# Kernel optimization log

Measured on AMD Instinct MI355X. Metric: run time of the kernel, lower is better.

The kernel has to match this reference:

```python
import jax, jax.numpy as jnp
import numpy as np

B, S, D, H = 2, 2048, 1024, 16
DH = D // H  # depth per head = 64


def setup_inputs() -> dict:
    key = jax.random.key(0)
    ks = jax.random.split(key, 5)
    sc = 0.02
    return {
        "x": jax.random.normal(ks[0], (B, S, D), dtype=jnp.float32),
        "Wq": jax.random.normal(ks[1], (D, D), dtype=jnp.float32) * sc,
        "bq": jnp.zeros((D,), dtype=jnp.float32),
        "Wk": jax.random.normal(ks[2], (D, D), dtype=jnp.float32) * sc,
        "bk": jnp.zeros((D,), dtype=jnp.float32),
        "Wv": jax.random.normal(ks[3], (D, D), dtype=jnp.float32) * sc,
        "bv": jnp.zeros((D,), dtype=jnp.float32),
        "Wo": jax.random.normal(ks[4], (D, D), dtype=jnp.float32) * sc,
        "bo": jnp.zeros((D,), dtype=jnp.float32),
    }


def _split_heads(t):
    # [B,S,D] -> [B,H,S,DH]
    return t.reshape(B, S, H, DH).transpose(0, 2, 1, 3)


def reference(x, Wq, bq, Wk, bk, Wv, bv, Wo, bo):
    q = _split_heads(x @ Wq + bq)
    k = _split_heads(x @ Wk + bk)
    v = _split_heads(x @ Wv + bv)
    scale = 1.0 / jnp.sqrt(jnp.float32(DH))
    logits = jnp.einsum("bhqd,bhkd->bhqk", q, k) * scale  # [B,H,S,S]
    attn = jax.nn.softmax(logits, axis=-1)
    ctx = jnp.einsum("bhqk,bhkd->bhqd", attn, v)
    ctx = ctx.transpose(0, 2, 1, 3).reshape(B, S, D)
    # dropout is identity at inference
    return ctx @ Wo + bo
```

## Files before the change

kernel.cpp:

```cpp
#include <hip/hip_runtime.h>
#include <hip/hip_bf16.h>

#define S_LEN   2048
#define D_MODEL 1024
#define NHEAD   16
#define DHEAD   64
#define M_ROWS  4096
#define BHEADS  32

typedef __attribute__((ext_vector_type(8)))  short short8;
typedef __attribute__((ext_vector_type(4)))  float f32x4;
typedef __attribute__((ext_vector_type(16))) float f32x16;
typedef __attribute__((ext_vector_type(4)))  unsigned short us4;

extern "C" __device__ float __ocml_native_exp2_f32(float);

__device__ __forceinline__ unsigned short f2b(float f) {
    unsigned int u = __builtin_bit_cast(unsigned int, f);
    return (unsigned short)((u + 0x7FFFu + ((u >> 16) & 1u)) >> 16);
}

__device__ __forceinline__ unsigned int pk2b(float lo, float hi) {
    unsigned int u0 = __builtin_bit_cast(unsigned int, lo) + 0x8000u;
    unsigned int u1 = __builtin_bit_cast(unsigned int, hi) + 0x8000u;
    return __builtin_amdgcn_perm(u1, u0, 0x07060302u);
}

#define GLOAD16(gp, lp) __builtin_amdgcn_global_load_lds(                     \
        (const __attribute__((address_space(1))) void*)(gp),                  \
        (__attribute__((address_space(3))) void*)(lp), 16, 0, 0)

#define STAGE_OFS(lane) ((((lane) & 3) ^ (((lane) >> 3) & 3)) * 8)

__global__ __launch_bounds__(256) void convert_x(
    const float* __restrict__ x, unsigned short* __restrict__ xb)
{
    const int i = (blockIdx.x * 256 + threadIdx.x) * 4;
    const float4 v = *(const float4*)&x[i];
    us4 o;
    o.x = f2b(v.x); o.y = f2b(v.y); o.z = f2b(v.z); o.w = f2b(v.w);
    *(us4*)&xb[i] = o;
}

__global__ __launch_bounds__(256) void transpose_w(
    const float* __restrict__ Wq, const float* __restrict__ Wk,
    const float* __restrict__ Wv, const float* __restrict__ Wo,
    unsigned short* __restrict__ Wqt, unsigned short* __restrict__ Wkt,
    unsigned short* __restrict__ Wvt, unsigned short* __restrict__ Wot)
{
    __shared__ float tile[32][33];
    const int z = blockIdx.z;
    const float* W = z == 0 ? Wq : (z == 1 ? Wk : (z == 2 ? Wv : Wo));
    unsigned short* Wt = z == 0 ? Wqt : (z == 1 ? Wkt : (z == 2 ? Wvt : Wot));
    const int tx = threadIdx.x, ty = threadIdx.y;
    const int n0 = blockIdx.x * 32, k0 = blockIdx.y * 32;
    #pragma unroll
    for (int i = 0; i < 4; ++i)
        tile[ty + i * 8][tx] = W[(size_t)(k0 + ty + i * 8) * D_MODEL + n0 + tx];
    __syncthreads();
    #pragma unroll
    for (int i = 0; i < 4; ++i)
        Wt[(size_t)(n0 + ty + i * 8) * D_MODEL + k0 + tx] = f2b(tile[tx][ty + i * 8]);
}

__global__ __launch_bounds__(256) void gemm_qkv(
    const unsigned short* __restrict__ xb,
    const unsigned short* __restrict__ Wqt, const unsigned short* __restrict__ Wkt,
    const unsigned short* __restrict__ Wvt,
    const float* __restrict__ bq, const float* __restrict__ bk,
    const float* __restrict__ bv,
    unsigned short* __restrict__ Qb, unsigned short* __restrict__ Kb,
    unsigned short* __restrict__ Vt)
{
    __shared__ unsigned short As[128][32];
    __shared__ unsigned short Bs[128][32];

    const int z = blockIdx.z;
    const unsigned short* Wt = z == 0 ? Wqt : (z == 1 ? Wkt : Wvt);
    const float* bias = z == 0 ? bq : (z == 1 ? bk : bv);

    const int t = threadIdx.x, lane = t & 63, w = t >> 6;
    const int wm = w >> 1, wn = w & 1;
    const int bm = blockIdx.y * 128, bn = blockIdx.x * 128;
    const int lr = lane >> 2, lc = STAGE_OFS(lane);
    const int lm = lane & 15, quad = lane >> 4;
    const int qo = (quad ^ ((lm >> 1) & 3)) * 8;

    f32x4 acc[4][4] = {};

    for (int kt = 0; kt < D_MODEL; kt += 32) {
        __syncthreads();
        #pragma unroll
        for (int i = 0; i < 2; ++i) {
            const int c = 2 * w + i;
            GLOAD16(xb + (size_t)(bm + c * 16 + lr) * D_MODEL + kt + lc, &As[c * 16][0]);
            GLOAD16(Wt + (size_t)(bn + c * 16 + lr) * D_MODEL + kt + lc, &Bs[c * 16][0]);
        }
        __syncthreads();

        short8 af[4], bfr[4];
        #pragma unroll
        for (int mi = 0; mi < 4; ++mi)
            af[mi] = *(const short8*)&As[wm * 64 + mi * 16 + lm][qo];
        #pragma unroll
        for (int ni = 0; ni < 4; ++ni)
            bfr[ni] = *(const short8*)&Bs[wn * 64 + ni * 16 + lm][qo];
        #pragma unroll
        for (int mi = 0; mi < 4; ++mi)
            #pragma unroll
            for (int ni = 0; ni < 4; ++ni)
                acc[mi][ni] = __builtin_amdgcn_mfma_f32_16x16x32_bf16(
                    af[mi], bfr[ni], acc[mi][ni], 0, 0, 0);
    }

    float bb[4];
    #pragma unroll
    for (int ni = 0; ni < 4; ++ni)
        bb[ni] = bias[bn + wn * 64 + ni * 16 + lm];
    const float scale = (z == 0) ? 0.18033688011112042f : 1.0f;

    if (z < 2) {
        unsigned short* Out = (z == 0) ? Qb : Kb;
        #pragma unroll
        for (int mi = 0; mi < 4; ++mi)
            #pragma unroll
            for (int r = 0; r < 4; ++r) {
                const int row = bm + wm * 64 + mi * 16 + quad * 4 + r;
                const int b = row >> 11, s = row & 2047;
                #pragma unroll
                for (int ni = 0; ni < 4; ++ni) {
                    const int col = bn + wn * 64 + ni * 16 + lm;
                    const int h = col >> 6, d = col & 63;
                    Out[(((size_t)(b * NHEAD + h)) * S_LEN + s) * DHEAD + d] =
                        f2b((acc[mi][ni][r] + bb[ni]) * scale);
                }
            }
    } else {
        #pragma unroll
        for (int mi = 0; mi < 4; ++mi) {
            const int row0 = bm + wm * 64 + mi * 16 + quad * 4;
            const int b = row0 >> 11, s0 = row0 & 2047;
            #pragma unroll
            for (int ni = 0; ni < 4; ++ni) {
                const int col = bn + wn * 64 + ni * 16 + lm;
                const int h = col >> 6, d = col & 63;
                us4 pk;
                pk.x = f2b(acc[mi][ni][0] + bb[ni]);
                pk.y = f2b(acc[mi][ni][1] + bb[ni]);
                pk.z = f2b(acc[mi][ni][2] + bb[ni]);
                pk.w = f2b(acc[mi][ni][3] + bb[ni]);
                *(us4*)&Vt[(((size_t)(b * NHEAD + h)) * DHEAD + d) * S_LEN + s0] = pk;
            }
        }
    }
}

__global__ __launch_bounds__(256) void gemm_out(
    const unsigned short* __restrict__ Ab, const unsigned short* __restrict__ Wot,
    const float* __restrict__ bo, float* __restrict__ out)
{
    __shared__ unsigned short As[64][32];
    __shared__ unsigned short Bs[128][32];

    const int t = threadIdx.x, lane = t & 63, w = t >> 6;
    const int wm = w & 1, wn = w >> 1;
    const int bm = blockIdx.y * 64, bn = blockIdx.x * 128;
    const int lr = lane >> 2, lc = STAGE_OFS(lane);
    const int lm = lane & 15, quad = lane >> 4;
    const int qo = (quad ^ ((lm >> 1) & 3)) * 8;

    f32x4 acc[2][4] = {};

    for (int kt = 0; kt < D_MODEL; kt += 32) {
        __syncthreads();
        GLOAD16(Ab + (size_t)(bm + w * 16 + lr) * D_MODEL + kt + lc, &As[w * 16][0]);
        #pragma unroll
        for (int i = 0; i < 2; ++i)
            GLOAD16(Wot + (size_t)(bn + w * 32 + i * 16 + lr) * D_MODEL + kt + lc,
                    &Bs[w * 32 + i * 16][0]);
        __syncthreads();

        short8 af[2], bfr[4];
        #pragma unroll
        for (int mi = 0; mi < 2; ++mi)
            af[mi] = *(const short8*)&As[wm * 32 + mi * 16 + lm][qo];
        #pragma unroll
        for (int ni = 0; ni < 4; ++ni)
            bfr[ni] = *(const short8*)&Bs[wn * 64 + ni * 16 + lm][qo];
        #pragma unroll
        for (int mi = 0; mi < 2; ++mi)
            #pragma unroll
            for (int ni = 0; ni < 4; ++ni)
                acc[mi][ni] = __builtin_amdgcn_mfma_f32_16x16x32_bf16(
                    af[mi], bfr[ni], acc[mi][ni], 0, 0, 0);
    }

    float bb[4];
    #pragma unroll
    for (int ni = 0; ni < 4; ++ni)
        bb[ni] = bo[bn + wn * 64 + ni * 16 + lm];

    #pragma unroll
    for (int mi = 0; mi < 2; ++mi)
        #pragma unroll
        for (int r = 0; r < 4; ++r) {
            const int row = bm + wm * 32 + mi * 16 + quad * 4 + r;
            #pragma unroll
            for (int ni = 0; ni < 4; ++ni) {
                const int col = bn + wn * 64 + ni * 16 + lm;
                out[(size_t)row * D_MODEL + col] = acc[mi][ni][r] + bb[ni];
            }
        }
}

__global__ __launch_bounds__(256) void attn_mfma(
    const unsigned short* __restrict__ Q, const unsigned short* __restrict__ K,
    const unsigned short* __restrict__ V, unsigned short* __restrict__ Cx)
{
    __shared__ unsigned short Qs[2][128][32];
    __shared__ unsigned short Ks[2][64][32];
    __shared__ unsigned short Vs[2][64][32];
    __shared__ unsigned int   Ps[4][32][36];

    const int t = threadIdx.x, lane = t & 63, w = t >> 6;
    const int q5 = lane & 31, hi = lane >> 5;
    const int lr = lane >> 2, lcs = STAGE_OFS(lane);
    const int q0 = blockIdx.x * 128, bh = blockIdx.y;
    const int sw = (q5 >> 1) & 3;
    int sbo[4];
    #pragma unroll
    for (int sb = 0; sb < 4; ++sb) sbo[sb] = (sb ^ sw) * 8;

    const unsigned short* Qh = Q + (size_t)bh * (S_LEN * DHEAD);
    const unsigned short* Kh = K + (size_t)bh * (S_LEN * DHEAD);
    const unsigned short* Vh = V + (size_t)bh * (DHEAD * S_LEN);

    #pragma unroll
    for (int i = 0; i < 2; ++i)
        #pragma unroll
        for (int c = 0; c < 2; ++c)
            GLOAD16(Qh + (size_t)(q0 + w * 32 + c * 16 + lr) * DHEAD + i * 32 + lcs,
                    &Qs[i][w * 32 + c * 16][0]);
    __syncthreads();

    short8 qf[4];
    #pragma unroll
    for (int c = 0; c < 4; ++c)
        qf[c] = *(const short8*)&Qs[c >> 1][w * 32 + q5][sbo[(c & 1) * 2 + hi]];

    f32x16 acc[2] = {};
    float2 l2a = {0.f, 0.f}, l2b = {0.f, 0.f};

    for (int kt = 0; kt < S_LEN; kt += 64) {
        __syncthreads();
        #pragma unroll
        for (int i = 0; i < 2; ++i) {
            GLOAD16(Kh + (size_t)(kt + w * 16 + lr) * DHEAD + i * 32 + lcs,
                    &Ks[i][w * 16][0]);
            GLOAD16(Vh + (size_t)(w * 16 + lr) * S_LEN + kt + i * 32 + lcs,
                    &Vs[i][w * 16][0]);
        }
        __syncthreads();

        f32x16 sf[2] = {};
        #pragma unroll
        for (int c = 0; c < 4; ++c) {
            #pragma unroll
            for (int mt = 0; mt < 2; ++mt) {
                const short8 kf =
                    *(const short8*)&Ks[c >> 1][mt * 32 + q5][sbo[(c & 1) * 2 + hi]];
                sf[mt] = __builtin_amdgcn_mfma_f32_32x32x16_bf16(kf, qf[c], sf[mt], 0, 0, 0);
            }
        }

        #pragma unroll
        for (int mt = 0; mt < 2; ++mt)
            #pragma unroll
            for (int g = 0; g < 4; ++g) {
                const float p0 = __ocml_native_exp2_f32(sf[mt][g * 4 + 0]);
                const float p1 = __ocml_native_exp2_f32(sf[mt][g * 4 + 1]);
                const float p2 = __ocml_native_exp2_f32(sf[mt][g * 4 + 2]);
                const float p3 = __ocml_native_exp2_f32(sf[mt][g * 4 + 3]);
                l2a.x += p0; l2a.y += p1;
                l2b.x += p2; l2b.y += p3;
                uint2 pk;
                pk.x = pk2b(p0, p1);
                pk.y = pk2b(p2, p3);
                *(uint2*)&Ps[w][q5][mt * 16 + g * 4 + hi * 2] = pk;
            }

        #pragma unroll
        for (int c = 0; c < 4; ++c) {
            const short8 pf = *(const short8*)&Ps[w][q5][c * 8 + hi * 4];
            #pragma unroll
            for (int nt = 0; nt < 2; ++nt) {
                const short8 vf =
                    *(const short8*)&Vs[c >> 1][nt * 32 + q5][sbo[(c & 1) * 2 + hi]];
                acc[nt] = __builtin_amdgcn_mfma_f32_32x32x16_bf16(pf, vf, acc[nt], 0, 0, 0);
            }
        }
    }

    float l_acc = (l2a.x + l2a.y) + (l2b.x + l2b.y);
    l_acc += __shfl_xor(l_acc, 32);
    const float inv = 1.f / l_acc;
    const int b = bh >> 4, h = bh & 15;
    #pragma unroll
    for (int reg = 0; reg < 16; ++reg) {
        const int row = (reg & 3) + 8 * (reg >> 2) + 4 * hi;
        const float invr = __shfl(inv, row);
        const int s = q0 + w * 32 + row;
        const size_t base = ((size_t)(b * S_LEN + s)) * D_MODEL + h * DHEAD;
        Cx[base + q5]      = f2b(acc[0][reg] * invr);
        Cx[base + 32 + q5] = f2b(acc[1][reg] * invr);
    }
}

extern "C" void kernel_launch(void* const* d_in, const int* in_sizes, int n_in,
                              void* d_out, int out_size, void* d_ws, size_t ws_size,
                              hipStream_t stream)
{
    const float* x  = (const float*)d_in[0];
    const float* Wq = (const float*)d_in[1];
    const float* bq = (const float*)d_in[2];
    const float* Wk = (const float*)d_in[3];
    const float* bk = (const float*)d_in[4];
    const float* Wv = (const float*)d_in[5];
    const float* bv = (const float*)d_in[6];
    const float* Wo = (const float*)d_in[7];
    const float* bo = (const float*)d_in[8];
    float* out = (float*)d_out;

    unsigned short* xb  = (unsigned short*)d_ws;
    unsigned short* Wqt = xb  + (size_t)M_ROWS * D_MODEL;
    unsigned short* Wkt = Wqt + (size_t)D_MODEL * D_MODEL;
    unsigned short* Wvt = Wkt + (size_t)D_MODEL * D_MODEL;
    unsigned short* Wot = Wvt + (size_t)D_MODEL * D_MODEL;
    unsigned short* Qb  = Wot + (size_t)D_MODEL * D_MODEL;
    unsigned short* Kb  = Qb  + (size_t)M_ROWS * D_MODEL;
    unsigned short* Vt  = Kb  + (size_t)M_ROWS * D_MODEL;
    unsigned short* Cxb = Vt  + (size_t)M_ROWS * D_MODEL;

    convert_x<<<dim3(M_ROWS * D_MODEL / 1024), dim3(256), 0, stream>>>(x, xb);
    transpose_w<<<dim3(32, 32, 4), dim3(32, 8), 0, stream>>>(
        Wq, Wk, Wv, Wo, Wqt, Wkt, Wvt, Wot);

    gemm_qkv<<<dim3(D_MODEL / 128, M_ROWS / 128, 3), dim3(256), 0, stream>>>(
        xb, Wqt, Wkt, Wvt, bq, bk, bv, Qb, Kb, Vt);

    attn_mfma<<<dim3(S_LEN / 128, BHEADS), dim3(256), 0, stream>>>(Qb, Kb, Vt, Cxb);

    gemm_out<<<dim3(D_MODEL / 128, M_ROWS / 64), dim3(256), 0, stream>>>(
        Cxb, Wot, bo, out);
}
```

Measured before the change: 210.1 us.

## Merge prep kernels and pass attention probabilities via lane shuffles instead of LDS

Folds the x-to-bf16 conversion into the weight transpose kernel as an extra grid slice, saving one kernel launch. In attention, the softmax probabilities are packed into registers and exchanged across half-waves with shuffles to form the PV MFMA operand. This removes the per-warp LDS buffer and its store/load round trip. Also adds a min-blocks-per-CU hint of 4 to the attention kernel, which could force register spilling.

```diff
diff --git a/kernel.cpp b/kernel.cpp
--- a/kernel.cpp
+++ b/kernel.cpp
@@ -32,27 +32,31 @@
 
 #define STAGE_OFS(lane) ((((lane) & 3) ^ (((lane) >> 3) & 3)) * 8)
 
-__global__ __launch_bounds__(256) void convert_x(
-    const float* __restrict__ x, unsigned short* __restrict__ xb)
-{
-    const int i = (blockIdx.x * 256 + threadIdx.x) * 4;
-    const float4 v = *(const float4*)&x[i];
-    us4 o;
-    o.x = f2b(v.x); o.y = f2b(v.y); o.z = f2b(v.z); o.w = f2b(v.w);
-    *(us4*)&xb[i] = o;
-}
-
-__global__ __launch_bounds__(256) void transpose_w(
+__global__ __launch_bounds__(256) void prep(
+    const float* __restrict__ x, unsigned short* __restrict__ xb,
     const float* __restrict__ Wq, const float* __restrict__ Wk,
     const float* __restrict__ Wv, const float* __restrict__ Wo,
     unsigned short* __restrict__ Wqt, unsigned short* __restrict__ Wkt,
     unsigned short* __restrict__ Wvt, unsigned short* __restrict__ Wot)
 {
+    const int z = blockIdx.z;
+    const int tx = threadIdx.x, ty = threadIdx.y;
+    if (z == 4) {
+        const int blk = blockIdx.y * 32 + blockIdx.x;
+        const int base = (blk * 256 + ty * 32 + tx) * 4;
+        #pragma unroll
+        for (int r = 0; r < 4; ++r) {
+            const int i = base + r * (M_ROWS * D_MODEL / 4);
+            const float4 v = *(const float4*)&x[i];
+            us4 o;
+            o.x = f2b(v.x); o.y = f2b(v.y); o.z = f2b(v.z); o.w = f2b(v.w);
+            *(us4*)&xb[i] = o;
+        }
+        return;
+    }
     __shared__ float tile[32][33];
-    const int z = blockIdx.z;
     const float* W = z == 0 ? Wq : (z == 1 ? Wk : (z == 2 ? Wv : Wo));
     unsigned short* Wt = z == 0 ? Wqt : (z == 1 ? Wkt : (z == 2 ? Wvt : Wot));
-    const int tx = threadIdx.x, ty = threadIdx.y;
     const int n0 = blockIdx.x * 32, k0 = blockIdx.y * 32;
     #pragma unroll
     for (int i = 0; i < 4; ++i)
@@ -213,14 +217,13 @@
         }
 }
 
-__global__ __launch_bounds__(256) void attn_mfma(
+__global__ __launch_bounds__(256, 4) void attn_mfma(
     const unsigned short* __restrict__ Q, const unsigned short* __restrict__ K,
     const unsigned short* __restrict__ V, unsigned short* __restrict__ Cx)
 {
     __shared__ unsigned short Qs[2][128][32];
     __shared__ unsigned short Ks[2][64][32];
     __shared__ unsigned short Vs[2][64][32];
-    __shared__ unsigned int   Ps[4][32][36];
 
     const int t = threadIdx.x, lane = t & 63, w = t >> 6;
     const int q5 = lane & 31, hi = lane >> 5;
@@ -274,29 +277,35 @@
         }
 
         #pragma unroll
-        for (int mt = 0; mt < 2; ++mt)
-            #pragma unroll
-            for (int g = 0; g < 4; ++g) {
-                const float p0 = __ocml_native_exp2_f32(sf[mt][g * 4 + 0]);
-                const float p1 = __ocml_native_exp2_f32(sf[mt][g * 4 + 1]);
-                const float p2 = __ocml_native_exp2_f32(sf[mt][g * 4 + 2]);
-                const float p3 = __ocml_native_exp2_f32(sf[mt][g * 4 + 3]);
+        for (int mt = 0; mt < 2; ++mt) {
+            unsigned int D[4][2];
+            #pragma unroll
+            for (int b = 0; b < 4; ++b) {
+                const float p0 = __ocml_native_exp2_f32(sf[mt][b * 4 + 0]);
+                const float p1 = __ocml_native_exp2_f32(sf[mt][b * 4 + 1]);
+                const float p2 = __ocml_native_exp2_f32(sf[mt][b * 4 + 2]);
+                const float p3 = __ocml_native_exp2_f32(sf[mt][b * 4 + 3]);
                 l2a.x += p0; l2a.y += p1;
                 l2b.x += p2; l2b.y += p3;
-                uint2 pk;
-                pk.x = pk2b(p0, p1);
-                pk.y = pk2b(p2, p3);
-                *(uint2*)&Ps[w][q5][mt * 16 + g * 4 + hi * 2] = pk;
-            }
-
-        #pragma unroll
-        for (int c = 0; c < 4; ++c) {
-            const short8 pf = *(const short8*)&Ps[w][q5][c * 8 + hi * 4];
-            #pragma unroll
-            for (int nt = 0; nt < 2; ++nt) {
-                const short8 vf =
-                    *(const short8*)&Vs[c >> 1][nt * 32 + q5][sbo[(c & 1) * 2 + hi]];
-                acc[nt] = __builtin_amdgcn_mfma_f32_32x32x16_bf16(pf, vf, acc[nt], 0, 0, 0);
+                D[b][0] = pk2b(p0, p1);
+                D[b][1] = pk2b(p2, p3);
+            }
+            #pragma unroll
+            for (int h01 = 0; h01 < 2; ++h01) {
+                const unsigned int sx0 = __shfl_xor(D[2 * h01 + (hi ^ 1)][0], 32);
+                const unsigned int sx1 = __shfl_xor(D[2 * h01 + (hi ^ 1)][1], 32);
+                uint4 fr;
+                fr.x = hi ? sx0 : D[2 * h01][0];
+                fr.y = hi ? sx1 : D[2 * h01][1];
+                fr.z = hi ? D[2 * h01 + 1][0] : sx0;
+                fr.w = hi ? D[2 * h01 + 1][1] : sx1;
+                const short8 pf = __builtin_bit_cast(short8, fr);
+                #pragma unroll
+                for (int nt = 0; nt < 2; ++nt) {
+                    const short8 vf =
+                        *(const short8*)&Vs[mt][nt * 32 + q5][sbo[h01 * 2 + hi]];
+                    acc[nt] = __builtin_amdgcn_mfma_f32_32x32x16_bf16(pf, vf, acc[nt], 0, 0, 0);
+                }
             }
         }
     }
@@ -341,9 +350,8 @@
     unsigned short* Vt  = Kb  + (size_t)M_ROWS * D_MODEL;
     unsigned short* Cxb = Vt  + (size_t)M_ROWS * D_MODEL;
 
-    convert_x<<<dim3(M_ROWS * D_MODEL / 1024), dim3(256), 0, stream>>>(x, xb);
-    transpose_w<<<dim3(32, 32, 4), dim3(32, 8), 0, stream>>>(
-        Wq, Wk, Wv, Wo, Wqt, Wkt, Wvt, Wot);
+    prep<<<dim3(32, 32, 5), dim3(32, 8), 0, stream>>>(
+        x, xb, Wq, Wk, Wv, Wo, Wqt, Wkt, Wvt, Wot);
 
     gemm_qkv<<<dim3(D_MODEL / 128, M_ROWS / 128, 3), dim3(256), 0, stream>>>(
         xb, Wqt, Wkt, Wvt, bq, bk, bv, Qb, Kb, Vt);
```

Result: slower. 218.1 us (+3.8%).

## Double-buffer LDS tiles in GEMMs and attention, merge prep kernels

Applied to the files above, without the earlier changes.

The two GEMM kernels and the attention kernel now double-buffer their shared-memory tiles. The next K-slice is issued with global_load_lds before the MFMAs on the current buffer run, and each iteration ends with one barrier instead of two. The x conversion and weight transposes are merged into one prep launch, using a fifth grid slice for x, to save one kernel launch. This doubles LDS use per block, which may cut occupancy. Correctness relies on the single end-of-iteration barrier also covering completion of the async LDS loads.

```diff
diff --git a/kernel.cpp b/kernel.cpp
--- a/kernel.cpp
+++ b/kernel.cpp
@@ -32,27 +32,31 @@
 
 #define STAGE_OFS(lane) ((((lane) & 3) ^ (((lane) >> 3) & 3)) * 8)
 
-__global__ __launch_bounds__(256) void convert_x(
-    const float* __restrict__ x, unsigned short* __restrict__ xb)
-{
-    const int i = (blockIdx.x * 256 + threadIdx.x) * 4;
-    const float4 v = *(const float4*)&x[i];
-    us4 o;
-    o.x = f2b(v.x); o.y = f2b(v.y); o.z = f2b(v.z); o.w = f2b(v.w);
-    *(us4*)&xb[i] = o;
-}
-
-__global__ __launch_bounds__(256) void transpose_w(
+__global__ __launch_bounds__(256) void prep(
+    const float* __restrict__ x, unsigned short* __restrict__ xb,
     const float* __restrict__ Wq, const float* __restrict__ Wk,
     const float* __restrict__ Wv, const float* __restrict__ Wo,
     unsigned short* __restrict__ Wqt, unsigned short* __restrict__ Wkt,
     unsigned short* __restrict__ Wvt, unsigned short* __restrict__ Wot)
 {
+    const int z = blockIdx.z;
+    const int tx = threadIdx.x, ty = threadIdx.y;
+    if (z == 4) {
+        const int blk = blockIdx.y * 32 + blockIdx.x;
+        const int base = (blk * 256 + ty * 32 + tx) * 4;
+        #pragma unroll
+        for (int r = 0; r < 4; ++r) {
+            const int i = base + r * (M_ROWS * D_MODEL / 4);
+            const float4 v = *(const float4*)&x[i];
+            us4 o;
+            o.x = f2b(v.x); o.y = f2b(v.y); o.z = f2b(v.z); o.w = f2b(v.w);
+            *(us4*)&xb[i] = o;
+        }
+        return;
+    }
     __shared__ float tile[32][33];
-    const int z = blockIdx.z;
     const float* W = z == 0 ? Wq : (z == 1 ? Wk : (z == 2 ? Wv : Wo));
     unsigned short* Wt = z == 0 ? Wqt : (z == 1 ? Wkt : (z == 2 ? Wvt : Wot));
-    const int tx = threadIdx.x, ty = threadIdx.y;
     const int n0 = blockIdx.x * 32, k0 = blockIdx.y * 32;
     #pragma unroll
     for (int i = 0; i < 4; ++i)
@@ -72,8 +76,8 @@
     unsigned short* __restrict__ Qb, unsigned short* __restrict__ Kb,
     unsigned short* __restrict__ Vt)
 {
-    __shared__ unsigned short As[128][32];
-    __shared__ unsigned short Bs[128][32];
+    __shared__ unsigned short As[2][128][32];
+    __shared__ unsigned short Bs[2][128][32];
 
     const int z = blockIdx.z;
     const unsigned short* Wt = z == 0 ? Wqt : (z == 1 ? Wkt : Wvt);
@@ -88,29 +92,43 @@
 
     f32x4 acc[4][4] = {};
 
-    for (int kt = 0; kt < D_MODEL; kt += 32) {
-        __syncthreads();
-        #pragma unroll
-        for (int i = 0; i < 2; ++i) {
-            const int c = 2 * w + i;
-            GLOAD16(xb + (size_t)(bm + c * 16 + lr) * D_MODEL + kt + lc, &As[c * 16][0]);
-            GLOAD16(Wt + (size_t)(bn + c * 16 + lr) * D_MODEL + kt + lc, &Bs[c * 16][0]);
-        }
-        __syncthreads();
+    #pragma unroll
+    for (int i = 0; i < 2; ++i) {
+        const int c = 2 * w + i;
+        GLOAD16(xb + (size_t)(bm + c * 16 + lr) * D_MODEL + lc, &As[0][c * 16][0]);
+        GLOAD16(Wt + (size_t)(bn + c * 16 + lr) * D_MODEL + lc, &Bs[0][c * 16][0]);
+    }
+    __syncthreads();
+
+    for (int it = 0; it < 32; ++it) {
+        const int cur = it & 1;
+        if (it + 1 < 32) {
+            const int kt = (it + 1) * 32;
+            #pragma unroll
+            for (int i = 0; i < 2; ++i) {
+                const int c = 2 * w + i;
+                GLOAD16(xb + (size_t)(bm + c * 16 + lr) * D_MODEL + kt + lc,
+                        &As[cur ^ 1][c * 16][0]);
+                GLOAD16(Wt + (size_t)(bn + c * 16 + lr) * D_MODEL + kt + lc,
+                        &Bs[cur ^ 1][c * 16][0]);
+            }
+        }
 
         short8 af[4], bfr[4];
         #pragma unroll
         for (int mi = 0; mi < 4; ++mi)
-            af[mi] = *(const short8*)&As[wm * 64 + mi * 16 + lm][qo];
+            af[mi] = *(const short8*)&As[cur][wm * 64 + mi * 16 + lm][qo];
         #pragma unroll
         for (int ni = 0; ni < 4; ++ni)
-            bfr[ni] = *(const short8*)&Bs[wn * 64 + ni * 16 + lm][qo];
+            bfr[ni] = *(const short8*)&Bs[cur][wn * 64 + ni * 16 + lm][qo];
         #pragma unroll
         for (int mi = 0; mi < 4; ++mi)
             #pragma unroll
             for (int ni = 0; ni < 4; ++ni)
                 acc[mi][ni] = __builtin_amdgcn_mfma_f32_16x16x32_bf16(
                     af[mi], bfr[ni], acc[mi][ni], 0, 0, 0);
+
+        __syncthreads();
     }
 
     float bb[4];
@@ -159,8 +177,8 @@
     const unsigned short* __restrict__ Ab, const unsigned short* __restrict__ Wot,
     const float* __restrict__ bo, float* __restrict__ out)
 {
-    __shared__ unsigned short As[64][32];
-    __shared__ unsigned short Bs[128][32];
+    __shared__ unsigned short As[2][64][32];
+    __shared__ unsigned short Bs[2][128][32];
 
     const int t = threadIdx.x, lane = t & 63, w = t >> 6;
     const int wm = w & 1, wn = w >> 1;
@@ -171,28 +189,40 @@
 
     f32x4 acc[2][4] = {};
 
-    for (int kt = 0; kt < D_MODEL; kt += 32) {
-        __syncthreads();
-        GLOAD16(Ab + (size_t)(bm + w * 16 + lr) * D_MODEL + kt + lc, &As[w * 16][0]);
-        #pragma unroll
-        for (int i = 0; i < 2; ++i)
-            GLOAD16(Wot + (size_t)(bn + w * 32 + i * 16 + lr) * D_MODEL + kt + lc,
-                    &Bs[w * 32 + i * 16][0]);
-        __syncthreads();
+    GLOAD16(Ab + (size_t)(bm + w * 16 + lr) * D_MODEL + lc, &As[0][w * 16][0]);
+    #pragma unroll
+    for (int i = 0; i < 2; ++i)
+        GLOAD16(Wot + (size_t)(bn + w * 32 + i * 16 + lr) * D_MODEL + lc,
+                &Bs[0][w * 32 + i * 16][0]);
+    __syncthreads();
+
+    for (int it = 0; it < 32; ++it) {
+        const int cur = it & 1;
+        if (it + 1 < 32) {
+            const int kt = (it + 1) * 32;
+            GLOAD16(Ab + (size_t)(bm + w * 16 + lr) * D_MODEL + kt + lc,
+                    &As[cur ^ 1][w * 16][0]);
+            #pragma unroll
+            for (int i = 0; i < 2; ++i)
+                GLOAD16(Wot + (size_t)(bn + w * 32 + i * 16 + lr) * D_MODEL + kt + lc,
+                        &Bs[cur ^ 1][w * 32 + i * 16][0]);
+        }
 
         short8 af[2], bfr[4];
         #pragma unroll
         for (int mi = 0; mi < 2; ++mi)
-            af[mi] = *(const short8*)&As[wm * 32 + mi * 16 + lm][qo];
+            af[mi] = *(const short8*)&As[cur][wm * 32 + mi * 16 + lm][qo];
         #pragma unroll
         for (int ni = 0; ni < 4; ++ni)
-            bfr[ni] = *(const short8*)&Bs[wn * 64 + ni * 16 + lm][qo];
+            bfr[ni] = *(const short8*)&Bs[cur][wn * 64 + ni * 16 + lm][qo];
         #pragma unroll
         for (int mi = 0; mi < 2; ++mi)
             #pragma unroll
             for (int ni = 0; ni < 4; ++ni)
                 acc[mi][ni] = __builtin_amdgcn_mfma_f32_16x16x32_bf16(
                     af[mi], bfr[ni], acc[mi][ni], 0, 0, 0);
+
+        __syncthreads();
     }
 
     float bb[4];
@@ -218,8 +248,8 @@
     const unsigned short* __restrict__ V, unsigned short* __restrict__ Cx)
 {
     __shared__ unsigned short Qs[2][128][32];
-    __shared__ unsigned short Ks[2][64][32];
-    __shared__ unsigned short Vs[2][64][32];
+    __shared__ unsigned short Ks[2][2][64][32];
+    __shared__ unsigned short Vs[2][2][64][32];
     __shared__ unsigned int   Ps[4][32][36];
 
     const int t = threadIdx.x, lane = t & 63, w = t >> 6;
@@ -241,6 +271,11 @@
         for (int c = 0; c < 2; ++c)
             GLOAD16(Qh + (size_t)(q0 + w * 32 + c * 16 + lr) * DHEAD + i * 32 + lcs,
                     &Qs[i][w * 32 + c * 16][0]);
+    #pragma unroll
+    for (int i = 0; i < 2; ++i) {
+        GLOAD16(Kh + (size_t)(w * 16 + lr) * DHEAD + i * 32 + lcs, &Ks[0][i][w * 16][0]);
+        GLOAD16(Vh + (size_t)(w * 16 + lr) * S_LEN + i * 32 + lcs, &Vs[0][i][w * 16][0]);
+    }
     __syncthreads();
 
     short8 qf[4];
@@ -251,16 +286,18 @@
     f32x16 acc[2] = {};
     float2 l2a = {0.f, 0.f}, l2b = {0.f, 0.f};
 
-    for (int kt = 0; kt < S_LEN; kt += 64) {
-        __syncthreads();
-        #pragma unroll
-        for (int i = 0; i < 2; ++i) {
-            GLOAD16(Kh + (size_t)(kt + w * 16 + lr) * DHEAD + i * 32 + lcs,
-                    &Ks[i][w * 16][0]);
-            GLOAD16(Vh + (size_t)(w * 16 + lr) * S_LEN + kt + i * 32 + lcs,
-                    &Vs[i][w * 16][0]);
-        }
-        __syncthreads();
+    for (int it = 0; it < 32; ++it) {
+        const int cur = it & 1;
+        if (it + 1 < 32) {
+            const int kt = (it + 1) * 64;
+            #pragma unroll
+            for (int i = 0; i < 2; ++i) {
+                GLOAD16(Kh + (size_t)(kt + w * 16 + lr) * DHEAD + i * 32 + lcs,
+                        &Ks[cur ^ 1][i][w * 16][0]);
+                GLOAD16(Vh + (size_t)(w * 16 + lr) * S_LEN + kt + i * 32 + lcs,
+                        &Vs[cur ^ 1][i][w * 16][0]);
+            }
+        }
 
         f32x16 sf[2] = {};
         #pragma unroll
@@ -268,7 +305,7 @@
             #pragma unroll
             for (int mt = 0; mt < 2; ++mt) {
                 const short8 kf =
-                    *(const short8*)&Ks[c >> 1][mt * 32 + q5][sbo[(c & 1) * 2 + hi]];
+                    *(const short8*)&Ks[cur][c >> 1][mt * 32 + q5][sbo[(c & 1) * 2 + hi]];
                 sf[mt] = __builtin_amdgcn_mfma_f32_32x32x16_bf16(kf, qf[c], sf[mt], 0, 0, 0);
             }
         }
@@ -295,10 +332,12 @@
             #pragma unroll
             for (int nt = 0; nt < 2; ++nt) {
                 const short8 vf =
-                    *(const short8*)&Vs[c >> 1][nt * 32 + q5][sbo[(c & 1) * 2 + hi]];
+                    *(const short8*)&Vs[cur][c >> 1][nt * 32 + q5][sbo[(c & 1) * 2 + hi]];
                 acc[nt] = __builtin_amdgcn_mfma_f32_32x32x16_bf16(pf, vf, acc[nt], 0, 0, 0);
             }
         }
+
+        __syncthreads();
     }
 
     float l_acc = (l2a.x + l2a.y) + (l2b.x + l2b.y);
@@ -341,9 +380,8 @@
     unsigned short* Vt  = Kb  + (size_t)M_ROWS * D_MODEL;
     unsigned short* Cxb = Vt  + (size_t)M_ROWS * D_MODEL;
 
-    convert_x<<<dim3(M_ROWS * D_MODEL / 1024), dim3(256), 0, stream>>>(x, xb);
-    transpose_w<<<dim3(32, 32, 4), dim3(32, 8), 0, stream>>>(
-        Wq, Wk, Wv, Wo, Wqt, Wkt, Wvt, Wot);
+    prep<<<dim3(32, 32, 5), dim3(32, 8), 0, stream>>>(
+        x, xb, Wq, Wk, Wv, Wo, Wqt, Wkt, Wvt, Wot);
 
     gemm_qkv<<<dim3(D_MODEL / 128, M_ROWS / 128, 3), dim3(256), 0, stream>>>(
         xb, Wqt, Wkt, Wvt, bq, bk, bv, Qb, Kb, Vt);
```

Result: no change. 210.5 us (+0.2%).
